# Performance work log

Hardware: AMD Instinct MI355X
Metric: run time of the kernel (lower is better)

The kernel has to match this reference:

```python
import jax, jax.numpy as jnp
import numpy as np

B, T, C, U = 256, 512, 256, 64  # batch, time, classes (incl. blank), label length
BLANK = C - 1                   # keras ctc_batch_cost: blank is last class
S = 2 * U + 1                   # extended label length (blanks interleaved)
NEG = -1e30                     # safe log-zero for fp32
EPS = 1e-7                      # keras.backend.epsilon()


def setup_inputs() -> dict:
    key = jax.random.key(0)
    k1, k2 = jax.random.split(key)
    # y_pred are softmax probabilities over time, as fed to ctc_batch_cost
    y_pred = jax.nn.softmax(jax.random.normal(k1, (B, T, C), dtype=jnp.float32), axis=-1)
    # labels exclude the blank index (values in [0, C-2]); all U positions valid
    y_true = jax.random.randint(k2, (B, U), 0, C - 1, dtype=jnp.int32)
    return {"y_true": y_true, "y_pred": y_pred}


def _ctc_loss(y_pred, y_true):
    # keras ctc_batch_cost computes loss on log(y_pred + eps)
    log_probs = jnp.log(y_pred + EPS)                      # [B, T, C]
    # extended label sequence: blank, l1, blank, l2, ..., blank
    ext = jnp.full((B, S), BLANK, dtype=y_true.dtype).at[:, 1::2].set(y_true)
    # gather per-state emission log-probs: lp_ext[b,t,s] = log_probs[b,t,ext[b,s]]
    lp_ext = jnp.take_along_axis(log_probs, ext[:, None, :].astype(jnp.int32), axis=2)  # [B,T,S]
    # skip transition (s-2 -> s) allowed iff ext[s] != blank and ext[s] != ext[s-2]
    ext_m2 = jnp.pad(ext[:, :-2], ((0, 0), (2, 0)), constant_values=-1)
    skip_ok = (ext != BLANK) & (ext != ext_m2)             # [B, S]

    # alpha_0: can start in state 0 (blank) or state 1 (first label)
    alpha0 = (jnp.full((B, S), NEG, dtype=jnp.float32)
              .at[:, 0].set(lp_ext[:, 0, 0])
              .at[:, 1].set(lp_ext[:, 0, 1]))

    def step(alpha, lp_t):
        a1 = jnp.pad(alpha[:, :-1], ((0, 0), (1, 0)), constant_values=NEG)
        a2 = jnp.pad(alpha[:, :-2], ((0, 0), (2, 0)), constant_values=NEG)
        a2 = jnp.where(skip_ok, a2, NEG)
        alpha = jnp.logaddexp(jnp.logaddexp(alpha, a1), a2) + lp_t
        return alpha, None

    lp_time_major = jnp.swapaxes(lp_ext, 0, 1)             # [T, B, S]
    alpha, _ = jax.lax.scan(step, alpha0, lp_time_major[1:])
    # terminate in last blank or last label
    loss = -jnp.logaddexp(alpha[:, -1], alpha[:, -2])      # [B]
    return loss[:, None]                                   # [B, 1] like ctc_batch_cost


def reference(y_true, y_pred):
    return _ctc_loss(y_pred, y_true)
```

## Files before the change

### kernel.cpp

```cpp
#include <hip/hip_runtime.h>


constexpr int B = 256, T = 512, C = 256, U = 64;
constexpr int CH = 16;
constexpr int NBUF = 3;
constexpr int NCHUNK = 32;
#define EPSF 1e-7f

__device__ __forceinline__ float dpp_wave_shr1(float x) {
    return __int_as_float(__builtin_amdgcn_update_dpp(
        0, __float_as_int(x), 0x138, 0xf, 0xf, true));
}

#define DPPMAX(ctrl)                                                      \
    {                                                                     \
        float x_ = __int_as_float(__builtin_amdgcn_update_dpp(            \
            0, __float_as_int(m_), (ctrl), 0xf, 0xf, true));              \
        m_ = fmaxf(m_, x_);                                               \
    }

#define RESCALE()                                                         \
    {                                                                     \
        float m_ = fmaxf(fmaxf(a_even, a_odd), a_top);                    \
        DPPMAX(0x111) DPPMAX(0x112) DPPMAX(0x114) DPPMAX(0x118)           \
        DPPMAX(0x142) DPPMAX(0x143)                                       \
        const float mx_ = __int_as_float(                                 \
            __builtin_amdgcn_readlane(__float_as_int(m_), 63));           \
        int e_ = (__float_as_int(mx_) >> 23) & 0xff;                      \
        int k_ = 187 - e_;                                                \
        k_ = k_ > 127 ? 127 : k_;                                         \
        const float s_ = __int_as_float((k_ + 127) << 23);                \
        a_even *= s_; a_odd *= s_; a_top *= s_;                           \
        esum += k_;                                                       \
    }

#define STAGE(cc)                                                          \
    {                                                                      \
        const int cs_ = (cc);                                              \
        float* lbase_ = &rows[cs_ % NBUF][0][0];                           \
        _Pragma("unroll")                                                  \
        for (int i = 0; i < CH; ++i) {                                     \
            int t = 1 + cs_ * CH + i;                                      \
            t = t < T ? t : T - 1;                                         \
            const float* g_ = rowp + (size_t)t * C + (lane << 2);          \
            __builtin_amdgcn_global_load_lds(                              \
                (const __attribute__((address_space(1))) void*)g_,         \
                (__attribute__((address_space(3))) void*)(lbase_ + i * C), \
                16, 0, 0);                                                 \
        }                                                                  \
    }

#define LDS_READ(cc)                                                       \
    {                                                                      \
        const int cr_ = (cc);                                              \
        float(*row_)[C] = rows[cr_ % NBUF];                                \
        _Pragma("unroll")                                                  \
        for (int i = 0; i < CH; ++i) {                                     \
            lab[i] = row_[i][label];                                       \
            blk[i] = row_[i][C - 1];                                       \
        }                                                                  \
    }

#define COMP_CHUNK(NSTEPS)                                                 \
    {                                                                      \
        _Pragma("unroll")                                                  \
        for (int i = 0; i < (NSTEPS); ++i) {                               \
            const float pb = blk[i] + EPSF;                                \
            const float pl = lab[i] + EPSF;                                \
            const float po = dpp_wave_shr1(a_odd);                         \
            const float skp = skip_ok ? po : 0.f;                          \
            const float ne = (a_even + po) * pb;                           \
            const float no = (a_odd + a_even + skp) * pl;                  \
            const float nt = (a_top + a_odd) * pb;                         \
            a_even = ne; a_odd = no; a_top = nt;                           \
            if (((1 + i) & 7) == 0) RESCALE();                             \
        }                                                                  \
    }

__global__ __launch_bounds__(64) void ctc_kernel(const int* __restrict__ y_true,
                                                 const float* __restrict__ y_pred,
                                                 float* __restrict__ out) {
    __shared__ float rows[NBUF][CH][C];
    const int b = blockIdx.x;
    const int lane = threadIdx.x;
    const int label = y_true[b * U + lane];
    const int label_prev = __shfl_up(label, 1);
    const bool skip_ok = (lane > 0) && (label != label_prev);
    const float* __restrict__ rowp = y_pred + (size_t)b * (T * C);

    float a_even, a_odd, a_top;
    {
        const float pb = rowp[C - 1] + EPSF;
        const float pl = rowp[label] + EPSF;
        a_even = (lane == 0) ? pb : 0.f;
        a_odd  = (lane == 0) ? pl : 0.f;
        a_top  = 0.f;
    }
    int esum = 0;

    STAGE(0);
    STAGE(1);
    STAGE(2);

    float lab[CH], blk[CH];

    for (int c = 0; c < 30; ++c) {
        asm volatile("s_waitcnt vmcnt(32)" ::: "memory");
        __builtin_amdgcn_sched_barrier(0);
        LDS_READ(c);
        asm volatile("s_waitcnt lgkmcnt(0)" ::: "memory");
        __builtin_amdgcn_sched_barrier(0);
        if (c <= 28) STAGE(c + 3);
        COMP_CHUNK(CH);
    }

    {
        asm volatile("s_waitcnt vmcnt(16)" ::: "memory");
        __builtin_amdgcn_sched_barrier(0);
        LDS_READ(30);
        COMP_CHUNK(CH);
    }
    {
        asm volatile("s_waitcnt vmcnt(0)" ::: "memory");
        __builtin_amdgcn_sched_barrier(0);
        LDS_READ(31);
        COMP_CHUNK(CH - 1);
    }

    if (lane == 63)
        out[b] = -logf(a_top + a_odd) + (float)esum * 0.69314718055994531f;
}

extern "C" void kernel_launch(void* const* d_in, const int* in_sizes, int n_in,
                              void* d_out, int out_size, void* d_ws, size_t ws_size,
                              hipStream_t stream) {
    const int* y_true   = (const int*)d_in[0];
    const float* y_pred = (const float*)d_in[1];
    float* out = (float*)d_out;
    hipLaunchKernelGGL(ctc_kernel, dim3(B), dim3(64), 0, stream,
                       y_true, y_pred, out);
}
```

Before: 193.9 us.

## Split loading across four waves with register staging and double-buffered LDS

The block grows from one wave to four. All four waves now fetch time-step rows into registers with inline-asm global loads, keeping four chunks in flight, and write them into a double-buffered LDS tile. Wave 0 alone gathers the label and blank probabilities and runs the serial alpha recurrence, with a block barrier per chunk. The aim is to take memory-issue work off the compute wave and raise memory-level parallelism, at the cost of a barrier every chunk and a more fragile hand-scheduled asm pipeline.

```diff
diff --git a/kernel.cpp b/kernel.cpp
--- a/kernel.cpp
+++ b/kernel.cpp
@@ -3,9 +3,11 @@
 
 constexpr int B = 256, T = 512, C = 256, U = 64;
 constexpr int CH = 16;
-constexpr int NBUF = 3;
-constexpr int NCHUNK = 32;
 #define EPSF 1e-7f
+
+typedef float f4 __attribute__((ext_vector_type(4)));
+
+#define LDSA(p) ((unsigned)(size_t)(__attribute__((address_space(3))) void*)(p))
 
 __device__ __forceinline__ float dpp_wave_shr1(float x) {
     return __int_as_float(__builtin_amdgcn_update_dpp(
@@ -34,32 +36,59 @@
         esum += k_;                                                       \
     }
 
-#define STAGE(cc)                                                          \
-    {                                                                      \
-        const int cs_ = (cc);                                              \
-        float* lbase_ = &rows[cs_ % NBUF][0][0];                           \
+#define GLD(dst, p)                                                        \
+    asm volatile("global_load_dwordx4 %0, %1, off" : "=&v"(dst) : "v"(p));
+
+#define ISSUE(cc, ST)                                                      \
+    {                                                                      \
+        const int c_ = (cc);                                               \
         _Pragma("unroll")                                                  \
-        for (int i = 0; i < CH; ++i) {                                     \
-            int t = 1 + cs_ * CH + i;                                      \
+        for (int j = 0; j < 4; ++j) {                                      \
+            int t = 1 + c_ * CH + rbase + j;                               \
             t = t < T ? t : T - 1;                                         \
-            const float* g_ = rowp + (size_t)t * C + (lane << 2);          \
-            __builtin_amdgcn_global_load_lds(                              \
-                (const __attribute__((address_space(1))) void*)g_,         \
-                (__attribute__((address_space(3))) void*)(lbase_ + i * C), \
-                16, 0, 0);                                                 \
+            const float* g_ = rowp + t * C + (lane << 2);                  \
+            GLD(ST[j], g_)                                                 \
         }                                                                  \
     }
 
-#define LDS_READ(cc)                                                       \
-    {                                                                      \
-        const int cr_ = (cc);                                              \
-        float(*row_)[C] = rows[cr_ % NBUF];                                \
-        _Pragma("unroll")                                                  \
-        for (int i = 0; i < CH; ++i) {                                     \
-            lab[i] = row_[i][label];                                       \
-            blk[i] = row_[i][C - 1];                                       \
-        }                                                                  \
-    }
+#define WRITE4(ST, WB)                                                     \
+    asm volatile("ds_write_b128 %0, %1" :: "v"(WB), "v"(ST[0]));           \
+    asm volatile("ds_write_b128 %0, %1 offset:1024" :: "v"(WB), "v"(ST[1]));\
+    asm volatile("ds_write_b128 %0, %1 offset:2048" :: "v"(WB), "v"(ST[2]));\
+    asm volatile("ds_write_b128 %0, %1 offset:3072" :: "v"(WB), "v"(ST[3]));
+
+#define VMC(N)                                                             \
+    asm volatile("s_waitcnt vmcnt(" #N ")" ::: "memory");                  \
+    __builtin_amdgcn_sched_barrier(0);
+
+#define DSR(dst, addr, OS)                                                 \
+    asm volatile("ds_read_b32 %0, %1 offset:" OS                           \
+                 : "=v"(dst) : "v"(addr));
+
+#define GATHER(LA, BA)                                                     \
+    {                                                                      \
+        DSR(lab[0],  LA, "0")     DSR(lab[1],  LA, "1024")                 \
+        DSR(lab[2],  LA, "2048")  DSR(lab[3],  LA, "3072")                 \
+        DSR(lab[4],  LA, "4096")  DSR(lab[5],  LA, "5120")                 \
+        DSR(lab[6],  LA, "6144")  DSR(lab[7],  LA, "7168")                 \
+        DSR(lab[8],  LA, "8192")  DSR(lab[9],  LA, "9216")                 \
+        DSR(lab[10], LA, "10240") DSR(lab[11], LA, "11264")                \
+        DSR(lab[12], LA, "12288") DSR(lab[13], LA, "13312")                \
+        DSR(lab[14], LA, "14336") DSR(lab[15], LA, "15360")                \
+        DSR(blk[0],  BA, "0")     DSR(blk[1],  BA, "1024")                 \
+        DSR(blk[2],  BA, "2048")  DSR(blk[3],  BA, "3072")                 \
+        DSR(blk[4],  BA, "4096")  DSR(blk[5],  BA, "5120")                 \
+        DSR(blk[6],  BA, "6144")  DSR(blk[7],  BA, "7168")                 \
+        DSR(blk[8],  BA, "8192")  DSR(blk[9],  BA, "9216")                 \
+        DSR(blk[10], BA, "10240") DSR(blk[11], BA, "11264")                \
+        DSR(blk[12], BA, "12288") DSR(blk[13], BA, "13312")                \
+        DSR(blk[14], BA, "14336") DSR(blk[15], BA, "15360")                \
+    }
+
+#define FENCE_BAR()                                                        \
+    asm volatile("s_waitcnt lgkmcnt(0)" ::: "memory");                     \
+    __builtin_amdgcn_sched_barrier(0);                                     \
+    __builtin_amdgcn_s_barrier();
 
 #define COMP_CHUNK(NSTEPS)                                                 \
     {                                                                      \
@@ -77,58 +106,89 @@
         }                                                                  \
     }
 
-__global__ __launch_bounds__(64) void ctc_kernel(const int* __restrict__ y_true,
-                                                 const float* __restrict__ y_pred,
-                                                 float* __restrict__ out) {
-    __shared__ float rows[NBUF][CH][C];
+#define ITER(cc, STI, STW, WB, LA, BA)                                     \
+    {                                                                      \
+        if (wid == 0) { GATHER(LA, BA) }                                   \
+        __builtin_amdgcn_sched_barrier(0);                                 \
+        ISSUE((cc) + 4, STI)                                               \
+        VMC(12)                                                            \
+        WRITE4(STW, WB)                                                    \
+        FENCE_BAR()                                                        \
+        if (wid == 0) { COMP_CHUNK(CH) }                                   \
+    }
+
+#define ITER_T(cc, NN, STW, WB, LA, BA)                                    \
+    {                                                                      \
+        if (wid == 0) { GATHER(LA, BA) }                                   \
+        __builtin_amdgcn_sched_barrier(0);                                 \
+        VMC(NN)                                                            \
+        WRITE4(STW, WB)                                                    \
+        FENCE_BAR()                                                        \
+        if (wid == 0) { COMP_CHUNK(CH) }                                   \
+    }
+
+__global__ __launch_bounds__(256) void ctc_kernel(const int* __restrict__ y_true,
+                                                  const float* __restrict__ y_pred,
+                                                  float* __restrict__ out) {
+    __shared__ float rows[2][CH][C];
     const int b = blockIdx.x;
-    const int lane = threadIdx.x;
+    const int tid = threadIdx.x;
+    const int lane = tid & 63;
+    const int wid = tid >> 6;
+    const int rbase = wid << 2;
+    const float* __restrict__ rowp = y_pred + (size_t)b * (T * C);
+
     const int label = y_true[b * U + lane];
     const int label_prev = __shfl_up(label, 1);
     const bool skip_ok = (lane > 0) && (label != label_prev);
-    const float* __restrict__ rowp = y_pred + (size_t)b * (T * C);
-
-    float a_even, a_odd, a_top;
-    {
+
+    float a_even = 0.f, a_odd = 0.f, a_top = 0.f;
+    int esum = 0;
+    float lab[CH], blk[CH];
+
+    if (wid == 0) {
         const float pb = rowp[C - 1] + EPSF;
         const float pl = rowp[label] + EPSF;
         a_even = (lane == 0) ? pb : 0.f;
         a_odd  = (lane == 0) ? pl : 0.f;
-        a_top  = 0.f;
-    }
-    int esum = 0;
-
-    STAGE(0);
-    STAGE(1);
-    STAGE(2);
-
-    float lab[CH], blk[CH];
-
-    for (int c = 0; c < 30; ++c) {
-        asm volatile("s_waitcnt vmcnt(32)" ::: "memory");
-        __builtin_amdgcn_sched_barrier(0);
-        LDS_READ(c);
+    }
+
+    const unsigned wb0 = LDSA(&rows[0][rbase][0]) + (lane << 4);
+    const unsigned wb1 = LDSA(&rows[1][rbase][0]) + (lane << 4);
+    const unsigned labA0 = LDSA(&rows[0][0][label]);
+    const unsigned labA1 = LDSA(&rows[1][0][label]);
+    const unsigned blkA0 = LDSA(&rows[0][0][C - 1]);
+    const unsigned blkA1 = LDSA(&rows[1][0][C - 1]);
+
+    f4 s0[4], s1[4], s2[4], s3[4];
+
+    asm volatile("s_waitcnt vmcnt(0)" ::: "memory");
+    __builtin_amdgcn_sched_barrier(0);
+
+    ISSUE(0, s0) ISSUE(1, s1) ISSUE(2, s2) ISSUE(3, s3)
+    VMC(12)
+    WRITE4(s0, wb0)
+    FENCE_BAR()
+
+    for (int q = 0; q < 7; ++q) {
+        const int c = q << 2;
+        ITER(c + 0, s0, s1, wb1, labA0, blkA0)
+        ITER(c + 1, s1, s2, wb0, labA1, blkA1)
+        ITER(c + 2, s2, s3, wb1, labA0, blkA0)
+        ITER(c + 3, s3, s0, wb0, labA1, blkA1)
+    }
+    ITER_T(28, 8, s1, wb1, labA0, blkA0)
+    ITER_T(29, 4, s2, wb0, labA1, blkA1)
+    ITER_T(30, 0, s3, wb1, labA0, blkA0)
+
+    if (wid == 0) {
+        GATHER(labA1, blkA1)
         asm volatile("s_waitcnt lgkmcnt(0)" ::: "memory");
         __builtin_amdgcn_sched_barrier(0);
-        if (c <= 28) STAGE(c + 3);
-        COMP_CHUNK(CH);
-    }
-
-    {
-        asm volatile("s_waitcnt vmcnt(16)" ::: "memory");
-        __builtin_amdgcn_sched_barrier(0);
-        LDS_READ(30);
-        COMP_CHUNK(CH);
-    }
-    {
-        asm volatile("s_waitcnt vmcnt(0)" ::: "memory");
-        __builtin_amdgcn_sched_barrier(0);
-        LDS_READ(31);
-        COMP_CHUNK(CH - 1);
-    }
-
-    if (lane == 63)
-        out[b] = -logf(a_top + a_odd) + (float)esum * 0.69314718055994531f;
+        COMP_CHUNK(CH - 1)
+        if (lane == 63)
+            out[b] = -logf(a_top + a_odd) + (float)esum * 0.69314718055994531f;
+    }
 }
 
 extern "C" void kernel_launch(void* const* d_in, const int* in_sizes, int n_in,
@@ -137,6 +197,6 @@
     const int* y_true   = (const int*)d_in[0];
     const float* y_pred = (const float*)d_in[1];
     float* out = (float*)d_out;
-    hipLaunchKernelGGL(ctc_kernel, dim3(B), dim3(64), 0, stream,
+    hipLaunchKernelGGL(ctc_kernel, dim3(B), dim3(256), 0, stream,
                        y_true, y_pred, out);
 }
```

Measured after the change: 195.5 us. No clear change (+0.9%).

## Split CTC into a parallel gather pre-pass and a compact recurrence kernel

Applied to the files above, without the earlier changes.

Adds a separate extract kernel that runs across 2048 blocks and gathers the per-label and blank probabilities into a compact workspace buffer of 66 floats per timestep. The serial recurrence kernel then reads only those compact rows, double-buffered in registers, instead of streaming full 256-class rows through LDS. The aim is to take the memory-bound gather off the latency-critical serial chain and to spread the full read of y_pred across many more blocks. The cost is an extra launch plus a workspace write and read, and the tail handling now relies on a per-step t<T guard.

```diff
diff --git a/kernel.cpp b/kernel.cpp
--- a/kernel.cpp
+++ b/kernel.cpp
@@ -2,10 +2,35 @@
 
 
 constexpr int B = 256, T = 512, C = 256, U = 64;
+constexpr int CS = 66;
 constexpr int CH = 16;
-constexpr int NBUF = 3;
-constexpr int NCHUNK = 32;
 #define EPSF 1e-7f
+
+__global__ __launch_bounds__(256) void ctc_extract(const int* __restrict__ y_true,
+                                                   const float* __restrict__ y_pred,
+                                                   float* __restrict__ cmp) {
+    __shared__ float buf[4][C];
+    const int g = blockIdx.x;
+    const int b = g >> 3;
+    const int t0 = (g & 7) << 6;
+    const int tid = threadIdx.x, lane = tid & 63, wid = tid >> 6;
+    const int label = y_true[b * U + lane];
+    const float* __restrict__ rp = y_pred + ((size_t)b * T + t0) * C;
+    float* __restrict__ cp = cmp + ((size_t)b * T + t0) * CS;
+
+    float4 v = *(const float4*)(rp + wid * C + (lane << 2));
+    for (int k = 0; k < 16; ++k) {
+        float4 vn = v;
+        if (k < 15)
+            vn = *(const float4*)(rp + (((k + 1) << 2) + wid) * C + (lane << 2));
+        *(float4*)(&buf[wid][lane << 2]) = v;
+        const int r = (k << 2) + wid;
+        float* crow = cp + r * CS;
+        crow[lane] = buf[wid][label];
+        if (lane == 0) crow[64] = buf[wid][C - 1];
+        v = vn;
+    }
+}
 
 __device__ __forceinline__ float dpp_wave_shr1(float x) {
     return __int_as_float(__builtin_amdgcn_update_dpp(
@@ -34,97 +59,71 @@
         esum += k_;                                                       \
     }
 
-#define STAGE(cc)                                                          \
-    {                                                                      \
-        const int cs_ = (cc);                                              \
-        float* lbase_ = &rows[cs_ % NBUF][0][0];                           \
-        _Pragma("unroll")                                                  \
-        for (int i = 0; i < CH; ++i) {                                     \
-            int t = 1 + cs_ * CH + i;                                      \
-            t = t < T ? t : T - 1;                                         \
-            const float* g_ = rowp + (size_t)t * C + (lane << 2);          \
-            __builtin_amdgcn_global_load_lds(                              \
-                (const __attribute__((address_space(1))) void*)g_,         \
-                (__attribute__((address_space(3))) void*)(lbase_ + i * C), \
-                16, 0, 0);                                                 \
-        }                                                                  \
+#define LOAD_CHUNK(LA, BL, cidx)                                          \
+    {                                                                     \
+        const int c_ = (cidx);                                            \
+        _Pragma("unroll")                                                 \
+        for (int i = 0; i < CH; ++i) {                                    \
+            int t = 1 + c_ * CH + i;                                      \
+            t = t < T ? t : T - 1;                                        \
+            LA[i] = labp[(size_t)t * CS];                                 \
+            BL[i] = blkp[(size_t)t * CS];                                 \
+        }                                                                 \
     }
 
-#define LDS_READ(cc)                                                       \
-    {                                                                      \
-        const int cr_ = (cc);                                              \
-        float(*row_)[C] = rows[cr_ % NBUF];                                \
-        _Pragma("unroll")                                                  \
-        for (int i = 0; i < CH; ++i) {                                     \
-            lab[i] = row_[i][label];                                       \
-            blk[i] = row_[i][C - 1];                                       \
-        }                                                                  \
-    }
-
-#define COMP_CHUNK(NSTEPS)                                                 \
-    {                                                                      \
-        _Pragma("unroll")                                                  \
-        for (int i = 0; i < (NSTEPS); ++i) {                               \
-            const float pb = blk[i] + EPSF;                                \
-            const float pl = lab[i] + EPSF;                                \
-            const float po = dpp_wave_shr1(a_odd);                         \
-            const float skp = skip_ok ? po : 0.f;                          \
-            const float ne = (a_even + po) * pb;                           \
-            const float no = (a_odd + a_even + skp) * pl;                  \
-            const float nt = (a_top + a_odd) * pb;                         \
-            a_even = ne; a_odd = no; a_top = nt;                           \
-            if (((1 + i) & 7) == 0) RESCALE();                             \
-        }                                                                  \
+#define COMP_CHUNK(LA, BL, cidx)                                          \
+    {                                                                     \
+        const int c_ = (cidx);                                            \
+        _Pragma("unroll")                                                 \
+        for (int i = 0; i < CH; ++i) {                                    \
+            const int t = 1 + c_ * CH + i;                                \
+            if (t < T) {                                                  \
+                const float pb = BL[i] + EPSF;                            \
+                const float pl = LA[i] + EPSF;                            \
+                const float po = dpp_wave_shr1(a_odd);                    \
+                const float skp = skip_ok ? po : 0.f;                     \
+                const float ne = (a_even + po) * pb;                      \
+                const float no = (a_odd + a_even + skp) * pl;             \
+                const float nt = (a_top + a_odd) * pb;                    \
+                a_even = ne; a_odd = no; a_top = nt;                      \
+                if ((t & 7) == 0) RESCALE();                              \
+            }                                                             \
+        }                                                                 \
     }
 
 __global__ __launch_bounds__(64) void ctc_kernel(const int* __restrict__ y_true,
-                                                 const float* __restrict__ y_pred,
+                                                 const float* __restrict__ cmp,
                                                  float* __restrict__ out) {
-    __shared__ float rows[NBUF][CH][C];
     const int b = blockIdx.x;
     const int lane = threadIdx.x;
     const int label = y_true[b * U + lane];
     const int label_prev = __shfl_up(label, 1);
     const bool skip_ok = (lane > 0) && (label != label_prev);
-    const float* __restrict__ rowp = y_pred + (size_t)b * (T * C);
+    const float* __restrict__ cmpb = cmp + (size_t)b * T * CS;
+    const float* __restrict__ labp = cmpb + lane;
+    const float* __restrict__ blkp = cmpb + 64;
 
     float a_even, a_odd, a_top;
     {
-        const float pb = rowp[C - 1] + EPSF;
-        const float pl = rowp[label] + EPSF;
+        const float pb = blkp[0] + EPSF;
+        const float pl = labp[0] + EPSF;
         a_even = (lane == 0) ? pb : 0.f;
         a_odd  = (lane == 0) ? pl : 0.f;
         a_top  = 0.f;
     }
     int esum = 0;
 
-    STAGE(0);
-    STAGE(1);
-    STAGE(2);
+    float la0[CH], bl0[CH], la1[CH], bl1[CH];
+    LOAD_CHUNK(la0, bl0, 0);
 
-    float lab[CH], blk[CH];
-
-    for (int c = 0; c < 30; ++c) {
-        asm volatile("s_waitcnt vmcnt(32)" ::: "memory");
+    for (int c2 = 0; c2 < 16; ++c2) {
+        const int c = 2 * c2;
+        LOAD_CHUNK(la1, bl1, c + 1);
         __builtin_amdgcn_sched_barrier(0);
-        LDS_READ(c);
-        asm volatile("s_waitcnt lgkmcnt(0)" ::: "memory");
+        COMP_CHUNK(la0, bl0, c);
+        if (c2 < 15) LOAD_CHUNK(la0, bl0, c + 2);
         __builtin_amdgcn_sched_barrier(0);
-        if (c <= 28) STAGE(c + 3);
-        COMP_CHUNK(CH);
-    }
-
-    {
-        asm volatile("s_waitcnt vmcnt(16)" ::: "memory");
-        __builtin_amdgcn_sched_barrier(0);
-        LDS_READ(30);
-        COMP_CHUNK(CH);
-    }
-    {
-        asm volatile("s_waitcnt vmcnt(0)" ::: "memory");
-        __builtin_amdgcn_sched_barrier(0);
-        LDS_READ(31);
-        COMP_CHUNK(CH - 1);
+        COMP_CHUNK(la1, bl1, c + 1);
     }
 
     if (lane == 63)
@@ -137,6 +136,9 @@
     const int* y_true   = (const int*)d_in[0];
     const float* y_pred = (const float*)d_in[1];
     float* out = (float*)d_out;
+    float* cmp = (float*)d_ws;
+    hipLaunchKernelGGL(ctc_extract, dim3(B * 8), dim3(256), 0, stream,
+                       y_true, y_pred, cmp);
     hipLaunchKernelGGL(ctc_kernel, dim3(B), dim3(64), 0, stream,
-                       y_true, y_pred, out);
+                       y_true, cmp, out);
 }
```

Result: slower. 229.4 us (+18.3%).
